# Performance work log

Hardware: AMD Instinct MI355X
Metric: run time of the kernel (lower is better)

Reference implementation:

```python
import jax, jax.numpy as jnp
import numpy as np

EMBED = 1024
HEADS = 16
HDIM = EMBED // HEADS


def setup_inputs() -> dict:
    key = jax.random.key(0)
    ks = jax.random.split(key, 7)
    N, T = 16, 1024
    s = 1.0 / np.sqrt(EMBED)
    X = jax.random.normal(ks[0], (N, T, EMBED), dtype=jnp.float32)
    mask = jax.random.randint(ks[1], (N, 1, T, T), 0, 2, dtype=jnp.int32)
    Wq = jax.random.normal(ks[2], (EMBED, EMBED), dtype=jnp.float32) * s
    Wk = jax.random.normal(ks[3], (EMBED, EMBED), dtype=jnp.float32) * s
    Wv = jax.random.normal(ks[4], (EMBED, EMBED), dtype=jnp.float32) * s
    Wo = jax.random.normal(ks[5], (EMBED, EMBED), dtype=jnp.float32) * s
    bo = jax.random.normal(ks[6], (EMBED,), dtype=jnp.float32) * 0.01
    return {"X": X, "mask": mask, "Wq": Wq, "Wk": Wk, "Wv": Wv, "Wo": Wo, "bo": bo}


def reference(X, mask, Wq, Wk, Wv, Wo, bo):
    N, T, K = X.shape
    # QKV projections (Linear with bias=False): y = x @ W^T
    def proj(W):
        y = jnp.einsum('btk,ok->bto', X, W)          # [N, T, K]
        return y.reshape(N, T, HEADS, HDIM).transpose(0, 2, 1, 3)  # [N, H, T, hd]
    q, k, v = proj(Wq), proj(Wk), proj(Wv)
    # scaled dot-product scores; note source scales by sqrt(embed_size), not sqrt(head_dim)
    scores = jnp.einsum('bhqd,bhkd->bhqk', q, k) / jnp.sqrt(jnp.float32(K))
    scores = jnp.where(mask == 0, jnp.float32(-1e20), scores)
    attn = jax.nn.softmax(scores, axis=-1)
    out = jnp.einsum('bhqk,bhkd->bhqd', attn, v)     # [N, H, T, hd]
    out = out.transpose(0, 2, 1, 3).reshape(N, T, K)  # [N, T, K]
    return jnp.einsum('btk,ok->bto', out, Wo) + bo
```

## Files before the change

kernel.cpp:

```cpp
#include <hip/hip_runtime.h>
#include <hip/hip_bf16.h>

#define EMBED 1024
#define TSEQ  1024
#define NB    16
#define NH    16
#define HD    64
#define MROWS (NB * TSEQ)

typedef __bf16 bf16x8 __attribute__((ext_vector_type(8)));
typedef float  f32x4  __attribute__((ext_vector_type(4)));

__device__ __forceinline__ unsigned int f2bf_bits(float x) {
    union { float f; unsigned int u; } v; v.f = x;
    unsigned int r = v.u + 0x7FFFu + ((v.u >> 16) & 1u);
    return r >> 16;
}

__device__ __forceinline__ int detect_bf16(const unsigned int* __restrict__ X) {
    __shared__ int s_cnt;
    if (threadIdx.x == 0) s_cnt = 0;
    __syncthreads();
    int c = 0;
    const int base = threadIdx.x * 16;
#pragma unroll
    for (int i = 0; i < 16; ++i) {
        unsigned int e = (X[base + i] >> 7) & 0xFFu;
        c += (e >= 100u && e <= 150u) ? 1 : 0;
    }
    atomicAdd(&s_cnt, c);
    __syncthreads();
    return s_cnt >= 2458;
}

__device__ __forceinline__ uint4 load8(const void* __restrict__ p, size_t eoff,
                                       int is_bf16) {
    if (is_bf16) {
        return *(const uint4*)((const __hip_bfloat16*)p + eoff);
    }
    const float* f = (const float*)p + eoff;
    float4 a = *(const float4*)f;
    float4 b = *(const float4*)(f + 4);
    uint4 r;
    r.x = f2bf_bits(a.x) | (f2bf_bits(a.y) << 16);
    r.y = f2bf_bits(a.z) | (f2bf_bits(a.w) << 16);
    r.z = f2bf_bits(b.x) | (f2bf_bits(b.y) << 16);
    r.w = f2bf_bits(b.z) | (f2bf_bits(b.w) << 16);
    return r;
}

__device__ __forceinline__ void gload16(const __hip_bfloat16* g,
                                        __hip_bfloat16* l) {
    __builtin_amdgcn_global_load_lds(
        (const __attribute__((address_space(1))) void*)g,
        (__attribute__((address_space(3))) void*)l, 16, 0, 0);
}

__global__ __launch_bounds__(256) void to_bf16(
    const void* __restrict__ src, __hip_bfloat16* __restrict__ dst,
    int n8, const unsigned int* __restrict__ det)
{
    const int isbf = detect_bf16(det);
    const int i = blockIdx.x * 256 + threadIdx.x;
    if (i < n8) *(uint4*)(dst + (size_t)i * 8) = load8(src, (size_t)i * 8, isbf);
}

__global__ __launch_bounds__(256) void pack_mask(
    const int* __restrict__ m, unsigned* __restrict__ bm, int n)
{
    const int i = blockIdx.x * 256 + threadIdx.x;
    const unsigned long long bal = __ballot(i < n && m[i] != 0);
    if ((threadIdx.x & 31) == 0 && i < n) {
        bm[i >> 5] = (unsigned)(((threadIdx.x & 63) < 32) ? bal : (bal >> 32));
    }
}

#define BK  64

template<int AD, int BD>
__global__ __launch_bounds__(256) void gemm_t(
    const void* __restrict__ A,
    const void* __restrict__ W,
    void* __restrict__ C,
    const void* __restrict__ bias,
    const unsigned int* __restrict__ Xdet,
    int a_flex, int out_mode, float cscale)
{
    const int isbf = detect_bf16(Xdet);
    const int a_bf = a_flex ? isbf : 1;

    __shared__ __hip_bfloat16 As[128 * BK];
    __shared__ __hip_bfloat16 Bs[128 * BK];

    const int tid  = threadIdx.x;
    const int lane = tid & 63;
    const int w    = tid >> 6;
    const int wm   = w & 1;
    const int wn   = w >> 1;
    const int m0   = blockIdx.x * 128;
    const int n0   = blockIdx.y * 128;

    const int srow = tid >> 3;
    const int scol = ((tid & 7) ^ (srow & 7)) * 8;

    f32x4 acc[4][4];
#pragma unroll
    for (int i = 0; i < 4; ++i)
#pragma unroll
        for (int j = 0; j < 4; ++j)
            acc[i][j] = (f32x4){0.f, 0.f, 0.f, 0.f};

    const int fr  = lane & 15;
    const int fq  = lane >> 4;
    const int frm = fr & 7;

    for (int k0 = 0; k0 < EMBED; k0 += BK) {
        uint4 ra[4], rb[4];
        if constexpr (!AD) {
#pragma unroll
            for (int j = 0; j < 4; ++j)
                ra[j] = load8(A, (size_t)(m0 + srow + 32 * j) * EMBED + scol + k0,
                              a_bf);
        }
        if constexpr (!BD) {
#pragma unroll
            for (int j = 0; j < 4; ++j)
                rb[j] = load8(W, (size_t)(n0 + srow + 32 * j) * EMBED + scol + k0,
                              isbf);
        }
        __syncthreads();
        if constexpr (AD) {
            const __hip_bfloat16* Ab =
                (const __hip_bfloat16*)A + (size_t)(m0 + srow) * EMBED + scol + k0;
#pragma unroll
            for (int j = 0; j < 4; ++j)
                gload16(Ab + (size_t)(32 * j) * EMBED, &As[tid * 8 + j * 2048]);
        } else {
#pragma unroll
            for (int j = 0; j < 4; ++j)
                *(uint4*)&As[tid * 8 + j * 2048] = ra[j];
        }
        if constexpr (BD) {
            const __hip_bfloat16* Wp =
                (const __hip_bfloat16*)W + (size_t)(n0 + srow) * EMBED + scol + k0;
#pragma unroll
            for (int j = 0; j < 4; ++j)
                gload16(Wp + (size_t)(32 * j) * EMBED, &Bs[tid * 8 + j * 2048]);
        } else {
#pragma unroll
            for (int j = 0; j < 4; ++j)
                *(uint4*)&Bs[tid * 8 + j * 2048] = rb[j];
        }
        __syncthreads();

#pragma unroll
        for (int kk = 0; kk < 2; ++kk) {
            const int cph = ((kk * 4 + fq) ^ frm) * 8;
            bf16x8 af[4], bfr[4];
#pragma unroll
            for (int i = 0; i < 4; ++i) {
                af[i]  = *(const bf16x8*)&As[(wm * 64 + i * 16 + fr) * BK + cph];
                bfr[i] = *(const bf16x8*)&Bs[(wn * 64 + i * 16 + fr) * BK + cph];
            }
#pragma unroll
            for (int i = 0; i < 4; ++i)
#pragma unroll
                for (int j = 0; j < 4; ++j)
                    acc[i][j] = __builtin_amdgcn_mfma_f32_16x16x32_bf16(
                        af[i], bfr[j], acc[i][j], 0, 0, 0);
        }
    }

    float bv[4] = {0.f, 0.f, 0.f, 0.f};
    if (bias != nullptr) {
#pragma unroll
        for (int j = 0; j < 4; ++j) {
            const int idx = n0 + wn * 64 + j * 16 + fr;
            bv[j] = isbf ? __bfloat162float(((const __hip_bfloat16*)bias)[idx])
                         : ((const float*)bias)[idx];
        }
    }

    if (out_mode == 2) {
#pragma unroll
        for (int i = 0; i < 4; ++i) {
            const int row = m0 + wm * 64 + i * 16 + fq * 4;
            const int bb = row >> 10, tt = row & 1023;
#pragma unroll
            for (int j = 0; j < 4; ++j) {
                const int col = n0 + wn * 64 + j * 16 + fr;
                const int hh = col >> 6, dd = col & 63;
                uint2 st;
                st.x = f2bf_bits(acc[i][j][0] * cscale) |
                       (f2bf_bits(acc[i][j][1] * cscale) << 16);
                st.y = f2bf_bits(acc[i][j][2] * cscale) |
                       (f2bf_bits(acc[i][j][3] * cscale) << 16);
                *(uint2*)&((__hip_bfloat16*)C)[
                    (((size_t)(bb * NH + hh) * HD + dd) * TSEQ) + tt] = st;
            }
        }
        return;
    }

    const int c_bf = (out_mode == 1) ? isbf : 1;
#pragma unroll
    for (int i = 0; i < 4; ++i) {
        const int row = m0 + wm * 64 + i * 16 + fq * 4;
#pragma unroll
        for (int j = 0; j < 4; ++j) {
            const int col = n0 + wn * 64 + j * 16 + fr;
#pragma unroll
            for (int r = 0; r < 4; ++r) {
                const size_t off = (size_t)(row + r) * EMBED + col;
                const float v = acc[i][j][r] * cscale + bv[j];
                if (c_bf) ((__hip_bfloat16*)C)[off] = __float2bfloat16(v);
                else      ((float*)C)[off] = v;
            }
        }
    }
}

#define QT  64
#define KTL 128
#define NT  (TSEQ / KTL)
#define KP  72
#define VP  136
#define PP  136

__global__ __launch_bounds__(256) void attn_mfma(
    const __hip_bfloat16* __restrict__ Q,
    const __hip_bfloat16* __restrict__ K,
    const __hip_bfloat16* __restrict__ Vt,
    const int* __restrict__ mask,
    const unsigned* __restrict__ bmask,
    __hip_bfloat16* __restrict__ O)
{
    __shared__ __hip_bfloat16 Ks[KTL * KP];
    __shared__ __hip_bfloat16 Vs[HD * VP];
    __shared__ __hip_bfloat16 Ps[4][16 * PP];

    const int tid  = threadIdx.x;
    const int lane = tid & 63;
    const int w    = tid >> 6;
    const int fr   = lane & 15;
    const int fq   = lane >> 4;
    const int qb = blockIdx.x, h = blockIdx.y, b = blockIdx.z;
    const int q0 = qb * QT;

    const __hip_bfloat16* qptr =
        Q + (size_t)(b * TSEQ + q0 + w * 16 + fr) * EMBED + h * HD + fq * 8;
    const bf16x8 qa0 = *(const bf16x8*)qptr;
    const bf16x8 qa1 = *(const bf16x8*)(qptr + 32);

    const unsigned* bmbase = bmask
        ? bmask + (size_t)(b * TSEQ + q0 + w * 16 + fq * 4) * (TSEQ / 32)
        : nullptr;

    float lS[4];
    f32x4 oacc[4];
#pragma unroll
    for (int r = 0; r < 4; ++r) lS[r] = 0.f;
#pragma unroll
    for (int dt = 0; dt < 4; ++dt) oacc[dt] = (f32x4){0.f, 0.f, 0.f, 0.f};

    for (int kt = 0; kt < NT; ++kt) {
        __syncthreads();
#pragma unroll
        for (int i = 0; i < 4; ++i) {
            const int cc  = tid + 256 * i;
            const int key = cc >> 3;
            const int dc  = (cc & 7) * 8;
            *(uint4*)&Ks[key * KP + dc] = *(const uint4*)(
                K + (size_t)(b * TSEQ + kt * KTL + key) * EMBED + h * HD + dc);
            const int d  = cc >> 4;
            const int kc = (cc & 15) * 8;
            *(uint4*)&Vs[d * VP + kc] = *(const uint4*)(
                Vt + ((size_t)(b * NH + h) * HD + d) * TSEQ + kt * KTL + kc);
        }
        __syncthreads();

        uint4 mw[4];
        int mvf[8][4];
        if (bmask) {
#pragma unroll
            for (int r = 0; r < 4; ++r)
                mw[r] = *(const uint4*)(bmbase + (size_t)r * (TSEQ / 32) + kt * 4);
        } else {
            const int* mbase = mask +
                (size_t)(b * TSEQ + q0 + w * 16 + fq * 4) * TSEQ + kt * KTL + fr;
#pragma unroll
            for (int t = 0; t < 8; ++t)
#pragma unroll
                for (int r = 0; r < 4; ++r)
                    mvf[t][r] = mbase[r * TSEQ + t * 16];
        }

        f32x4 s[8];
#pragma unroll
        for (int t = 0; t < 8; ++t) {
            const bf16x8 kb0 = *(const bf16x8*)&Ks[(t * 16 + fr) * KP + fq * 8];
            const bf16x8 kb1 = *(const bf16x8*)&Ks[(t * 16 + fr) * KP + 32 + fq * 8];
            s[t] = __builtin_amdgcn_mfma_f32_16x16x32_bf16(
                qa0, kb0, (f32x4){0.f, 0.f, 0.f, 0.f}, 0, 0, 0);
            s[t] = __builtin_amdgcn_mfma_f32_16x16x32_bf16(qa1, kb1, s[t], 0, 0, 0);
        }

        if (bmask) {
#pragma unroll
            for (int t = 0; t < 8; ++t)
#pragma unroll
                for (int r = 0; r < 4; ++r) {
                    const unsigned wv = ((const unsigned*)&mw[r])[t >> 1] >> fr;
                    if (((wv >> ((t & 1) * 16)) & 1u) == 0u) s[t][r] = -1e30f;
                }
        } else {
#pragma unroll
            for (int t = 0; t < 8; ++t)
#pragma unroll
                for (int r = 0; r < 4; ++r)
                    if (mvf[t][r] == 0) s[t][r] = -1e30f;
        }

#pragma unroll
        for (int r = 0; r < 4; ++r) {
            float ls = 0.f;
#pragma unroll
            for (int t = 0; t < 8; ++t) {
                const float p = __builtin_amdgcn_exp2f(s[t][r]);
                s[t][r] = p;
                ls += p;
            }
            lS[r] += ls;
        }

#pragma unroll
        for (int t = 0; t < 8; ++t)
#pragma unroll
            for (int r = 0; r < 4; ++r)
                Ps[w][(fq * 4 + r) * PP + t * 16 + fr] = __float2bfloat16(s[t][r]);

#pragma unroll
        for (int kc = 0; kc < 4; ++kc) {
            const bf16x8 pa = *(const bf16x8*)&Ps[w][fr * PP + kc * 32 + fq * 8];
#pragma unroll
            for (int dt = 0; dt < 4; ++dt) {
                const bf16x8 vb =
                    *(const bf16x8*)&Vs[(dt * 16 + fr) * VP + kc * 32 + fq * 8];
                oacc[dt] = __builtin_amdgcn_mfma_f32_16x16x32_bf16(
                    pa, vb, oacc[dt], 0, 0, 0);
            }
        }
    }

    float inv[4];
#pragma unroll
    for (int r = 0; r < 4; ++r) {
#pragma unroll
        for (int off = 8; off > 0; off >>= 1) lS[r] += __shfl_xor(lS[r], off);
        inv[r] = 1.f / fmaxf(lS[r], 1e-30f);
    }
#pragma unroll
    for (int dt = 0; dt < 4; ++dt)
#pragma unroll
        for (int r = 0; r < 4; ++r)
            O[(size_t)(b * TSEQ + q0 + w * 16 + fq * 4 + r) * EMBED
              + h * HD + dt * 16 + fr] = __float2bfloat16(oacc[dt][r] * inv[r]);
}

static inline void launch_gemm(int ad, int bd, dim3 g, dim3 b, hipStream_t s,
                               const void* A, const void* W, void* C,
                               const void* bias, const unsigned int* Xdet,
                               int a_flex, int out_mode, float cs)
{
    if (ad && bd)
        gemm_t<1, 1><<<g, b, 0, s>>>(A, W, C, bias, Xdet, a_flex, out_mode, cs);
    else if (ad)
        gemm_t<1, 0><<<g, b, 0, s>>>(A, W, C, bias, Xdet, a_flex, out_mode, cs);
    else if (bd)
        gemm_t<0, 1><<<g, b, 0, s>>>(A, W, C, bias, Xdet, a_flex, out_mode, cs);
    else
        gemm_t<0, 0><<<g, b, 0, s>>>(A, W, C, bias, Xdet, a_flex, out_mode, cs);
}

extern "C" void kernel_launch(void* const* d_in, const int* in_sizes, int n_in,
                              void* d_out, int out_size, void* d_ws, size_t ws_size,
                              hipStream_t stream) {
    const void* X  = d_in[0];
    const int*  Mk = (const int*)d_in[1];
    const void* Wsrc[4] = { d_in[2], d_in[3], d_in[4], d_in[5] };
    const void* bo = d_in[6];
    const unsigned int* Xdet = (const unsigned int*)d_in[0];

    const size_t n_elem = (size_t)MROWS * EMBED;
    const size_t w_elem = (size_t)EMBED * EMBED;
    __hip_bfloat16* Qb  = (__hip_bfloat16*)d_ws;
    __hip_bfloat16* Kb  = Qb + n_elem;
    __hip_bfloat16* Vtb = (__hip_bfloat16*)d_out;
    size_t ws_used = 2 * n_elem * sizeof(__hip_bfloat16);

    dim3 blk(256);

    const void* Ax = X;
    int ad = 0;
    if (in_sizes[0] == (int)(n_elem * 2)) {
        ad = 1;
    } else {
        __hip_bfloat16* Xb = nullptr;
        if ((size_t)out_size >= n_elem * 4) {
            Xb = (__hip_bfloat16*)d_out + n_elem;
        } else if (ws_size >= ws_used + n_elem * 2) {
            Xb = (__hip_bfloat16*)((char*)d_ws + ws_used);
            ws_used += n_elem * 2;
        }
        if (Xb) {
            to_bf16<<<dim3((unsigned)(n_elem / 8 / 256)), blk, 0, stream>>>(
                X, Xb, (int)(n_elem / 8), Xdet);
            Ax = Xb;
            ad = 1;
        }
    }

    const void* Wb[4];
    int bd = 0;
    if (in_sizes[2] == (int)(w_elem * 2)) {
        for (int i = 0; i < 4; ++i) Wb[i] = Wsrc[i];
        bd = 1;
    } else if (ws_size >= ws_used + 4 * w_elem * 2) {
        __hip_bfloat16* p = (__hip_bfloat16*)((char*)d_ws + ws_used);
        for (int i = 0; i < 4; ++i) {
            to_bf16<<<dim3((unsigned)(w_elem / 8 / 256)), blk, 0, stream>>>(
                Wsrc[i], p + (size_t)i * w_elem, (int)(w_elem / 8), Xdet);
            Wb[i] = p + (size_t)i * w_elem;
        }
        ws_used += 4 * w_elem * 2;
        bd = 1;
    } else {
        for (int i = 0; i < 4; ++i) Wb[i] = Wsrc[i];
    }

    const size_t bm_words = (size_t)NB * TSEQ * (TSEQ / 32);
    const size_t bm_bytes = bm_words * 4;
    unsigned* bm = nullptr;
    if ((size_t)out_size >= n_elem * 2 + bm_bytes) {
        bm = (unsigned*)((char*)d_out + n_elem * 2);
    } else if (ws_size >= ws_used + bm_bytes) {
        bm = (unsigned*)((char*)d_ws + ws_used);
        ws_used += bm_bytes;
    }

    dim3 gg(MROWS / 128, EMBED / 128, 1);
    const float qs = 0.03125f * 1.44269504088896f;
    launch_gemm(ad, bd, gg, blk, stream, Ax, Wb[0], Qb,  nullptr, Xdet, 1, 0, qs);
    launch_gemm(ad, bd, gg, blk, stream, Ax, Wb[1], Kb,  nullptr, Xdet, 1, 0, 1.f);
    launch_gemm(ad, bd, gg, blk, stream, Ax, Wb[2], Vtb, nullptr, Xdet, 1, 2, 1.f);

    if (bm) {
        const int nmask = NB * TSEQ * TSEQ;
        pack_mask<<<dim3(nmask / 256), blk, 0, stream>>>(Mk, bm, nmask);
    }

    dim3 ga(TSEQ / QT, NH, NB);
    attn_mfma<<<ga, blk, 0, stream>>>(Qb, Kb, Vtb, Mk, bm, Qb);

    launch_gemm(1, bd, gg, blk, stream, Qb, Wb[3], d_out, bo, Xdet, 0, 1, 1.f);
}
```

Measured before the change: 568.7 us.

## Add 256x256 double-buffered bf16 GEMM kernel for projections when inputs are pre-converted

```diff
diff --git a/kernel.cpp b/kernel.cpp
--- a/kernel.cpp
+++ b/kernel.cpp
@@ -22,7 +22,7 @@
     if (threadIdx.x == 0) s_cnt = 0;
     __syncthreads();
     int c = 0;
-    const int base = threadIdx.x * 16;
+    const int base = (threadIdx.x & 255) * 16;
 #pragma unroll
     for (int i = 0; i < 16; ++i) {
         unsigned int e = (X[base + i] >> 7) & 0xFFu;
@@ -30,7 +30,7 @@
     }
     atomicAdd(&s_cnt, c);
     __syncthreads();
-    return s_cnt >= 2458;
+    return s_cnt >= (int)(0.6f * 16 * blockDim.x);
 }
 
 __device__ __forceinline__ uint4 load8(const void* __restrict__ p, size_t eoff,
@@ -76,6 +76,137 @@
 }
 
 #define BK  64
+
+#define NK2 (EMBED / BK)
+
+__global__ __launch_bounds__(512) void gemm256(
+    const __hip_bfloat16* __restrict__ A,
+    const __hip_bfloat16* __restrict__ W,
+    void* __restrict__ C,
+    const void* __restrict__ bias,
+    const unsigned int* __restrict__ Xdet,
+    int out_mode, float cscale)
+{
+    const int isbf = (out_mode == 1) ? detect_bf16(Xdet) : 1;
+
+    __shared__ __hip_bfloat16 As[2][256 * BK];
+    __shared__ __hip_bfloat16 Bs[2][256 * BK];
+
+    const int tid  = threadIdx.x;
+    const int lane = tid & 63;
+    const int w    = tid >> 6;
+    const int wm   = w & 1;
+    const int wn   = w >> 1;
+    const int m0   = blockIdx.x * 256;
+    const int n0   = blockIdx.y * 256;
+
+    const int srow = tid >> 3;
+    const int scol = ((tid & 7) ^ (srow & 7)) * 8;
+
+    const int fr  = lane & 15;
+    const int fq  = lane >> 4;
+    const int frm = fr & 7;
+
+    f32x4 acc[8][4];
+#pragma unroll
+    for (int i = 0; i < 8; ++i)
+#pragma unroll
+        for (int j = 0; j < 4; ++j)
+            acc[i][j] = (f32x4){0.f, 0.f, 0.f, 0.f};
+
+    const __hip_bfloat16* Ab = A + (size_t)(m0 + srow) * EMBED + scol;
+    const __hip_bfloat16* Wp = W + (size_t)(n0 + srow) * EMBED + scol;
+
+#pragma unroll
+    for (int j = 0; j < 4; ++j) {
+        gload16(Ab + (size_t)(64 * j) * EMBED, &As[0][tid * 8 + j * 4096]);
+        gload16(Wp + (size_t)(64 * j) * EMBED, &Bs[0][tid * 8 + j * 4096]);
+    }
+    __syncthreads();
+
+    int cur = 0;
+    for (int t = 0; t < NK2; ++t) {
+        if (t + 1 < NK2) {
+            const int k1 = (t + 1) * BK;
+#pragma unroll
+            for (int j = 0; j < 4; ++j) {
+                gload16(Ab + (size_t)(64 * j) * EMBED + k1,
+                        &As[cur ^ 1][tid * 8 + j * 4096]);
+                gload16(Wp + (size_t)(64 * j) * EMBED + k1,
+                        &Bs[cur ^ 1][tid * 8 + j * 4096]);
+            }
+        }
+#pragma unroll
+        for (int kk = 0; kk < 2; ++kk) {
+            const int cph = ((kk * 4 + fq) ^ frm) * 8;
+            bf16x8 af[8], bv8[4];
+#pragma unroll
+            for (int i = 0; i < 8; ++i)
+                af[i] = *(const bf16x8*)
+                    &As[cur][(wm * 128 + i * 16 + fr) * BK + cph];
+#pragma unroll
+            for (int j = 0; j < 4; ++j)
+                bv8[j] = *(const bf16x8*)
+                    &Bs[cur][(wn * 64 + j * 16 + fr) * BK + cph];
+#pragma unroll
+            for (int i = 0; i < 8; ++i)
+#pragma unroll
+                for (int j = 0; j < 4; ++j)
+                    acc[i][j] = __builtin_amdgcn_mfma_f32_16x16x32_bf16(
+                        af[i], bv8[j], acc[i][j], 0, 0, 0);
+        }
+        if (t + 1 < NK2) __syncthreads();
+        cur ^= 1;
+    }
+
+    float bv[4] = {0.f, 0.f, 0.f, 0.f};
+    if (bias != nullptr) {
+#pragma unroll
+        for (int j = 0; j < 4; ++j) {
+            const int idx = n0 + wn * 64 + j * 16 + fr;
+            bv[j] = isbf ? __bfloat162float(((const __hip_bfloat16*)bias)[idx])
+                         : ((const float*)bias)[idx];
+        }
+    }
+
+    if (out_mode == 2) {
+#pragma unroll
+        for (int i = 0; i < 8; ++i) {
+            const int row = m0 + wm * 128 + i * 16 + fq * 4;
+            const int bb = row >> 10, tt = row & 1023;
+#pragma unroll
+            for (int j = 0; j < 4; ++j) {
+                const int col = n0 + wn * 64 + j * 16 + fr;
+                const int hh = col >> 6, dd = col & 63;
+                uint2 st;
+                st.x = f2bf_bits(acc[i][j][0] * cscale) |
+                       (f2bf_bits(acc[i][j][1] * cscale) << 16);
+                st.y = f2bf_bits(acc[i][j][2] * cscale) |
+                       (f2bf_bits(acc[i][j][3] * cscale) << 16);
+                *(uint2*)&((__hip_bfloat16*)C)[
+                    (((size_t)(bb * NH + hh) * HD + dd) * TSEQ) + tt] = st;
+            }
+        }
+        return;
+    }
+
+    const int c_bf = (out_mode == 1) ? isbf : 1;
+#pragma unroll
+    for (int i = 0; i < 8; ++i) {
+        const int row = m0 + wm * 128 + i * 16 + fq * 4;
+#pragma unroll
+        for (int j = 0; j < 4; ++j) {
+            const int col = n0 + wn * 64 + j * 16 + fr;
+#pragma unroll
+            for (int r = 0; r < 4; ++r) {
+                const size_t off = (size_t)(row + r) * EMBED + col;
+                const float v = acc[i][j][r] * cscale + bv[j];
+                if (c_bf) ((__hip_bfloat16*)C)[off] = __float2bfloat16(v);
+                else      ((float*)C)[off] = v;
+            }
+        }
+    }
+}
 
 template<int AD, int BD>
 __global__ __launch_bounds__(256) void gemm_t(
@@ -448,11 +579,27 @@
         ws_used += bm_bytes;
     }
 
-    dim3 gg(MROWS / 128, EMBED / 128, 1);
     const float qs = 0.03125f * 1.44269504088896f;
-    launch_gemm(ad, bd, gg, blk, stream, Ax, Wb[0], Qb,  nullptr, Xdet, 1, 0, qs);
-    launch_gemm(ad, bd, gg, blk, stream, Ax, Wb[1], Kb,  nullptr, Xdet, 1, 0, 1.f);
-    launch_gemm(ad, bd, gg, blk, stream, Ax, Wb[2], Vtb, nullptr, Xdet, 1, 2, 1.f);
+    const int fast = ad && bd;
+
+    if (fast) {
+        dim3 blk5(512);
+        dim3 g2(MROWS / 256, EMBED / 256, 1);
+        gemm256<<<g2, blk5, 0, stream>>>(
+            (const __hip_bfloat16*)Ax, (const __hip_bfloat16*)Wb[0], Qb,
+            nullptr, Xdet, 0, qs);
+        gemm256<<<g2, blk5, 0, stream>>>(
+            (const __hip_bfloat16*)Ax, (const __hip_bfloat16*)Wb[1], Kb,
+            nullptr, Xdet, 0, 1.f);
+        gemm256<<<g2, blk5, 0, stream>>>(
+            (const __hip_bfloat16*)Ax, (const __hip_bfloat16*)Wb[2], Vtb,
+            nullptr, Xdet, 2, 1.f);
+    } else {
+        dim3 gg(MROWS / 128, EMBED / 128, 1);
+        launch_gemm(ad, bd, gg, blk, stream, Ax, Wb[0], Qb,  nullptr, Xdet, 1, 0, qs);
+        launch_gemm(ad, bd, gg, blk, stream, Ax, Wb[1], Kb,  nullptr, Xdet, 1, 0, 1.f);
+        launch_gemm(ad, bd, gg, blk, stream, Ax, Wb[2], Vtb, nullptr, Xdet, 1, 2, 1.f);
+    }
 
     if (bm) {
         const int nmask = NB * TSEQ * TSEQ;
@@ -462,5 +609,13 @@
     dim3 ga(TSEQ / QT, NH, NB);
     attn_mfma<<<ga, blk, 0, stream>>>(Qb, Kb, Vtb, Mk, bm, Qb);
 
-    launch_gemm(1, bd, gg, blk, stream, Qb, Wb[3], d_out, bo, Xdet, 0, 1, 1.f);
-}
+    if (fast) {
+        dim3 blk5(512);
+        dim3 g2(MROWS / 256, EMBED / 256, 1);
+        gemm256<<<g2, blk5, 0, stream>>>(
+            Qb, (const __hip_bfloat16*)Wb[3], d_out, bo, Xdet, 1, 1.f);
+    } else {
+        dim3 gg(MROWS / 128, EMBED / 128, 1);
+        launch_gemm(1, bd, gg, blk, stream, Qb, Wb[3], d_out, bo, Xdet, 0, 1, 1.f);
+    }
+}
```

Measured after the change: 553.2 us. 2.7% less time.
